# Kernel optimization log

Measured on AMD Instinct MI355X. Metric: run time of the kernel, lower is better.

Reference implementation:

```python
import jax, jax.numpy as jnp
import numpy as np

HEAD_SIZE = 64
BLOCK_SIZE = 4096
BATCH = 4


def setup_inputs() -> dict:
    key = jax.random.key(0)
    kx, kk, kq, kv = jax.random.split(key, 4)
    x = jax.random.normal(kx, (BATCH, BLOCK_SIZE, HEAD_SIZE), dtype=jnp.float32)
    s = HEAD_SIZE ** -0.5  # ~ torch default linear init scale
    Wk = jax.random.uniform(kk, (HEAD_SIZE, HEAD_SIZE), jnp.float32, -s, s)
    Wq = jax.random.uniform(kq, (HEAD_SIZE, HEAD_SIZE), jnp.float32, -s, s)
    Wv = jax.random.uniform(kv, (HEAD_SIZE, HEAD_SIZE), jnp.float32, -s, s)
    return {"x": x, "Wk": Wk, "Wq": Wq, "Wv": Wv}


def reference(x, Wk, Wq, Wv):
    # x: [B, T, C]; W*: [C, C] stored torch-style (out, in) -> y = x @ W.T
    B, T, C = x.shape
    k = x @ Wk.T  # [B, T, C]
    q = x @ Wq.T
    v = x @ Wv.T
    scores = jnp.einsum('btc,bsc->bts', q, k) * (C ** -0.5)  # [B, T, T]
    causal = jnp.tril(jnp.ones((T, T), dtype=bool))
    scores = jnp.where(causal, scores, -jnp.inf)
    weights = jax.nn.softmax(scores, axis=-1)
    out = jnp.einsum('bts,bsc->btc', weights, v)  # [B, T, C]
    return out
```

## Files before the change

### kernel.cpp

```cpp
#include <hip/hip_runtime.h>
#include <hip/hip_bf16.h>

typedef unsigned short u16;
typedef unsigned int u32;
typedef __bf16 bf16x8_t __attribute__((ext_vector_type(8)));
typedef float f32x4_t __attribute__((ext_vector_type(4)));
typedef float f32x16 __attribute__((ext_vector_type(16)));

constexpr int Bb = 4;
constexpr int Tt = 4096;
constexpr int Dd = 64;
constexpr float QSCALE = 0.18033688011112042f;

__device__ __forceinline__ u16 f2bf(float f) {
  unsigned int u = __builtin_bit_cast(unsigned int, f);
  return (u16)((u + 0x7fffu + ((u >> 16) & 1u)) >> 16);
}
__device__ __forceinline__ u32 pk2(float a, float b) {
  return (u32)f2bf(a) | ((u32)f2bf(b) << 16);
}
__device__ __forceinline__ u32 pkt(float a, float b) {
  const u32 ua = __builtin_bit_cast(u32, a);
  const u32 ub = __builtin_bit_cast(u32, b);
  return (ua >> 16) | (ub & 0xFFFF0000u);
}
__device__ __forceinline__ bf16x8_t ld16(const u16* p) {
  int4 v = *(const int4*)p;
  return __builtin_bit_cast(bf16x8_t, v);
}
__device__ __forceinline__ f32x4_t mfma16(bf16x8_t a, bf16x8_t b, f32x4_t c) {
  return __builtin_amdgcn_mfma_f32_16x16x32_bf16(a, b, c, 0, 0, 0);
}
__device__ __forceinline__ f32x16 mfma32(bf16x8_t a, bf16x8_t b, f32x16 c) {
  return __builtin_amdgcn_mfma_f32_32x32x16_bf16(a, b, c, 0, 0, 0);
}

__global__ __launch_bounds__(256) void HeadV1_proj(
    const float* __restrict__ x, const float* __restrict__ Wk,
    const float* __restrict__ Wq, const float* __restrict__ Wv,
    u16* __restrict__ qS, u16* __restrict__ kS, u16* __restrict__ vS)
{
  __shared__ u16 xl[64][72];
  __shared__ u16 Wl[3][64][72];
  __shared__ u16 ylds[64][72];

  const int t = threadIdx.x;
  const int w = t >> 6, lane = t & 63, l15 = lane & 15, quad = lane >> 4;
  const int r0 = blockIdx.x * 64;
  const int b  = r0 >> 12;
  const int kt = (r0 & 4095) >> 6;
  const long tilebase = ((long)(b * 64 + kt)) * 4096;

  {
    const float* srcs[4] = {x + (long)r0 * 64, Wk, Wq, Wv};
    u16* dstl[4] = {&xl[0][0], &Wl[0][0][0], &Wl[1][0][0], &Wl[2][0][0]};
    #pragma unroll
    for (int mm = 0; mm < 4; mm++) {
      const float* s = srcs[mm];
      u16* d = dstl[mm];
      #pragma unroll
      for (int i = 0; i < 4; i++) {
        const int f4 = i * 256 + t;
        const int row = f4 >> 4, c4 = f4 & 15;
        float4 v = ((const float4*)(s + row * 64))[c4];
        uint2 pk;
        pk.x = pk2(v.x, v.y);
        pk.y = pk2(v.z, v.w);
        *(uint2*)(d + row * 72 + c4 * 4) = pk;
      }
    }
  }
  __syncthreads();

  bf16x8_t xf[2];
  #pragma unroll
  for (int kh = 0; kh < 2; kh++)
    xf[kh] = ld16(&xl[w * 16 + l15][kh * 32 + quad * 8]);

  u16* dsts[3];
  dsts[0] = kS + tilebase; dsts[1] = qS + tilebase; dsts[2] = vS + tilebase;

  #pragma unroll
  for (int m = 0; m < 3; m++) {
    float vals[4][4];
    #pragma unroll
    for (int g = 0; g < 4; g++) {
      f32x4_t acc = {0.f, 0.f, 0.f, 0.f};
      #pragma unroll
      for (int kh = 0; kh < 2; kh++) {
        bf16x8_t wf = ld16(&Wl[m][g * 16 + l15][kh * 32 + quad * 8]);
        acc = mfma16(xf[kh], wf, acc);
      }
      #pragma unroll
      for (int r = 0; r < 4; r++)
        vals[g][r] = (m == 1) ? acc[r] * QSCALE : acc[r];
    }
    #pragma unroll
    for (int g = 0; g < 4; g++)
      #pragma unroll
      for (int r = 0; r < 4; r++)
        ylds[w * 16 + quad * 4 + r][g * 16 + l15] = f2bf(vals[g][r]);
    __syncthreads();
    if (m < 2) {
      #pragma unroll
      for (int kk = 0; kk < 2; kk++) {
        bf16x8_t f = ld16(&ylds[w * 16 + l15][kk * 32 + quad * 8]);
        *(int4*)(dsts[m] + (w * 2 + kk) * 512 + lane * 8) = __builtin_bit_cast(int4, f);
      }
    } else {
      #pragma unroll
      for (int kk = 0; kk < 2; kk++) {
        u16 tmp[8];
        #pragma unroll
        for (int j = 0; j < 8; j++)
          tmp[j] = ylds[kk * 32 + quad * 8 + j][w * 16 + l15];
        *(int4*)(dsts[2] + (kk * 4 + w) * 512 + lane * 8) = *(const int4*)tmp;
      }
    }
    __syncthreads();
  }
}

__global__ __launch_bounds__(1024, 4) void HeadV1_flash(
    const u16* __restrict__ qS, const u16* __restrict__ kS,
    const u16* __restrict__ vS, float* __restrict__ outg)
{
  __shared__ __align__(16) char smem[55296];
  float (*chk)[16][33]  = (float (*)[16][33])smem;
  float (*stg)[32][68]  = (float (*)[32][68])(smem + 33792);
  float (*lst)[2][32]   = (float (*)[2][32])(smem + 51200);

  const int t    = threadIdx.x;
  const int w    = t >> 6;
  const int lane = t & 63;
  const int l15  = lane & 15;
  const int lhb  = lane >> 5;
  const int l4   = (lane >> 4) & 1;
  const int q31  = lane & 31;

  const int xcd = blockIdx.x & 7;
  const int b   = xcd >> 1;
  const int i   = ((blockIdx.x >> 3) << 1) | (xcd & 1);
  const int j1 = i, j2 = 127 - i;
  const int nk1 = (j1 >> 1) + 1;
  const int nk2 = (j2 >> 1) + 1;
  int n1 = (16 * nk1 + 32) / 65;
  if (n1 < 1) n1 = 1;
  if (n1 > 15) n1 = 15;

  const bool grp2 = (w >= n1);
  const int j   = grp2 ? j2 : j1;
  const int nk  = grp2 ? nk2 : nk1;
  const int str = grp2 ? (16 - n1) : n1;
  const int off = grp2 ? (w - n1) : w;

  const int qt64 = j >> 1;
  const int ql0  = (j & 1) * 32;
  const int qr0  = j * 32;
  const long base = (long)b * Tt * Dd;

  const u16* qt_ = qS + ((long)(b * 64 + qt64)) * 4096;
  bf16x8_t qfrag[4];
  #pragma unroll
  for (int dsl = 0; dsl < 4; dsl++)
    qfrag[dsl] = ld16(qt_ + (((ql0 >> 4) + l4) * 2 + (dsl >> 1)) * 512
                          + (((dsl * 2 + lhb) & 3) * 16 + l15) * 8);

  f32x16 O0 = {0.f,0.f,0.f,0.f,0.f,0.f,0.f,0.f,0.f,0.f,0.f,0.f,0.f,0.f,0.f,0.f};
  f32x16 O1 = O0;
  float Lp = 0.f;

  const u16* kb = kS + ((long)(b * 64)) * 4096;
  const u16* vb = vS + ((long)(b * 64)) * 4096;

  for (int kt = off; kt < nk; kt += str) {
    const bool ismask = (kt == nk - 1);
    const u16* ktile = kb + (long)kt * 4096;
    const u16* vtile = vb + (long)kt * 4096;
    const int nh = (ismask && !(j & 1)) ? 1 : 2;

    for (int h2 = 0; h2 < nh; h2++) {
      bf16x8_t kf[4];
      #pragma unroll
      for (int dsl = 0; dsl < 4; dsl++)
        kf[dsl] = ld16(ktile + ((h2 * 2 + l4) * 2 + (dsl >> 1)) * 512
                             + (((dsl * 2 + lhb) & 3) * 16 + l15) * 8);
      bf16x8_t vf[2][2];
      #pragma unroll
      for (int ksl = 0; ksl < 2; ksl++)
        #pragma unroll
        for (int dh = 0; dh < 2; dh++)
          vf[ksl][dh] = ld16(vtile + (h2 * 4 + dh * 2 + l4) * 512
                                   + ((ksl * 2 + lhb) * 16 + l15) * 8);

      f32x16 S = {0.f,0.f,0.f,0.f,0.f,0.f,0.f,0.f,0.f,0.f,0.f,0.f,0.f,0.f,0.f,0.f};
      #pragma unroll
      for (int dsl = 0; dsl < 4; dsl++)
        S = mfma32(kf[dsl], qfrag[dsl], S);

      if (ismask && h2 == (j & 1)) {
        const int kvb = kt * 64 + h2 * 32 + 4 * lhb;
        const int qi  = qr0 + q31;
        #pragma unroll
        for (int r = 0; r < 16; r++) {
          const int kvg = kvb + (r & 3) + 8 * (r >> 2);
          if (kvg > qi) S[r] = -1e30f;
        }
      }

      float p[16];
      #pragma unroll
      for (int r = 0; r < 16; r++) p[r] = __builtin_amdgcn_exp2f(S[r]);
      #pragma unroll
      for (int r = 0; r < 16; r++) {
        const u32 u = __builtin_bit_cast(u32, p[r]) & 0xFFFF0000u;
        Lp += __builtin_bit_cast(float, u);
      }

      #pragma unroll
      for (int ksl = 0; ksl < 2; ksl++) {
        const u32 a0 = pkt(p[8 * ksl + 0], p[8 * ksl + 1]);
        const u32 a1 = pkt(p[8 * ksl + 2], p[8 * ksl + 3]);
        const u32 a2 = pkt(p[8 * ksl + 4], p[8 * ksl + 5]);
        const u32 a3 = pkt(p[8 * ksl + 6], p[8 * ksl + 7]);
        const u32 x02 = (u32)__shfl_xor((int)(lhb ? a0 : a2), 32);
        const u32 x13 = (u32)__shfl_xor((int)(lhb ? a1 : a3), 32);
        uint4 bw;
        bw.x = lhb ? x02 : a0;
        bw.y = lhb ? x13 : a1;
        bw.z = lhb ? a2 : x02;
        bw.w = lhb ? a3 : x13;
        const bf16x8_t Bf = __builtin_bit_cast(bf16x8_t, bw);
        __builtin_amdgcn_s_setprio(1);
        O0 = mfma32(vf[ksl][0], Bf, O0);
        O1 = mfma32(vf[ksl][1], Bf, O1);
        __builtin_amdgcn_s_setprio(0);
      }
    }
  }

  lst[w][lhb][q31] = Lp;
  __syncthreads();

  #pragma unroll
  for (int rr = 0; rr < 4; rr++) {
    #pragma unroll
    for (int rs = 0; rs < 8; rs++) {
      const int dloc = (rs & 3) + 8 * (rs >> 2) + 4 * lhb;
      const float val = (rr >> 1) ? ((rr & 1) ? O1[8 + rs] : O1[rs])
                                  : ((rr & 1) ? O0[8 + rs] : O0[rs]);
      chk[w][dloc][q31] = val;
    }
    __syncthreads();
    {
      const int jsel = t >> 9, tt = t & 511;
      const int d2 = tt >> 5, q = tt & 31;
      const int lo = jsel ? n1 : 0, hi = jsel ? 16 : n1;
      float s = 0.f;
      for (int w2 = lo; w2 < hi; w2++) s += chk[w2][d2][q];
      stg[jsel][q][rr * 16 + d2] = s;
    }
    __syncthreads();
  }

  {
    const int jsel = t >> 9, tt = t & 511;
    const int q = tt >> 4, dg = tt & 15;
    const int lo = jsel ? n1 : 0, hi = jsel ? 16 : n1;
    float L = 0.f;
    for (int w2 = lo; w2 < hi; w2++) L += lst[w2][0][q] + lst[w2][1][q];
    const float invL = 1.0f / L;
    const int jj = jsel ? j2 : j1;
    float4 v = *(const float4*)&stg[jsel][q][dg * 4];
    v.x *= invL; v.y *= invL; v.z *= invL; v.w *= invL;
    *(float4*)(outg + base + (long)(jj * 32 + q) * 64 + dg * 4) = v;
  }
}

extern "C" void kernel_launch(void* const* d_in, const int* in_sizes, int n_in,
                              void* d_out, int out_size, void* d_ws, size_t ws_size,
                              hipStream_t stream) {
  (void)in_sizes; (void)n_in; (void)out_size; (void)ws_size;
  const float* x  = (const float*)d_in[0];
  const float* Wk = (const float*)d_in[1];
  const float* Wq = (const float*)d_in[2];
  const float* Wv = (const float*)d_in[3];
  float* out = (float*)d_out;
  u16* qw  = (u16*)d_ws;
  u16* kw  = qw + (size_t)Bb * Tt * Dd;
  u16* vw  = kw + (size_t)Bb * Tt * Dd;

  HeadV1_proj<<<(Bb * Tt) / 64, 256, 0, stream>>>(x, Wk, Wq, Wv, qw, kw, vw);
  HeadV1_flash<<<256, 1024, 0, stream>>>(qw, kw, vw, out);
}
```

Measured before the change: 83.13 us.

## Compute softmax row sums via MFMA with ones and parallelize projection across 12 waves

The flash kernel no longer accumulates the softmax denominator with per-element VALU adds. It runs an extra 32x32 MFMA of a bf16 ones matrix against the packed probability fragment, which yields row sums already reduced across lanes, and the final reduction reads only one half. The projection kernel now launches 1024 threads so that three groups of four waves compute K, Q and V in parallel, each into its own LDS tile, removing the serial loop over matrices and its barriers. The cost is one extra MFMA per ksl step in the hot loop, plus four idle waves and more LDS in the projection blocks.

```diff
diff --git a/kernel.cpp b/kernel.cpp
--- a/kernel.cpp
+++ b/kernel.cpp
@@ -35,89 +35,86 @@
   return __builtin_amdgcn_mfma_f32_32x32x16_bf16(a, b, c, 0, 0, 0);
 }
 
-__global__ __launch_bounds__(256) void HeadV1_proj(
+__global__ __launch_bounds__(1024) void HeadV1_proj(
     const float* __restrict__ x, const float* __restrict__ Wk,
     const float* __restrict__ Wq, const float* __restrict__ Wv,
     u16* __restrict__ qS, u16* __restrict__ kS, u16* __restrict__ vS)
 {
   __shared__ u16 xl[64][72];
   __shared__ u16 Wl[3][64][72];
-  __shared__ u16 ylds[64][72];
+  __shared__ u16 yl[3][64][72];
 
   const int t = threadIdx.x;
   const int w = t >> 6, lane = t & 63, l15 = lane & 15, quad = lane >> 4;
-  const int r0 = blockIdx.x * 64;
-  const int b  = r0 >> 12;
-  const int kt = (r0 & 4095) >> 6;
+  const int blk = blockIdx.x;
+  const int r0 = blk * 64;
+  const int b  = blk >> 6;
+  const int kt = blk & 63;
   const long tilebase = ((long)(b * 64 + kt)) * 4096;
 
   {
     const float* srcs[4] = {x + (long)r0 * 64, Wk, Wq, Wv};
     u16* dstl[4] = {&xl[0][0], &Wl[0][0][0], &Wl[1][0][0], &Wl[2][0][0]};
+    const int row = t >> 4, c4 = t & 15;
     #pragma unroll
     for (int mm = 0; mm < 4; mm++) {
-      const float* s = srcs[mm];
-      u16* d = dstl[mm];
-      #pragma unroll
-      for (int i = 0; i < 4; i++) {
-        const int f4 = i * 256 + t;
-        const int row = f4 >> 4, c4 = f4 & 15;
-        float4 v = ((const float4*)(s + row * 64))[c4];
-        uint2 pk;
-        pk.x = pk2(v.x, v.y);
-        pk.y = pk2(v.z, v.w);
-        *(uint2*)(d + row * 72 + c4 * 4) = pk;
-      }
+      float4 v = ((const float4*)(srcs[mm] + row * 64))[c4];
+      uint2 pk;
+      pk.x = pk2(v.x, v.y);
+      pk.y = pk2(v.z, v.w);
+      *(uint2*)(dstl[mm] + row * 72 + c4 * 4) = pk;
     }
   }
   __syncthreads();
 
-  bf16x8_t xf[2];
-  #pragma unroll
-  for (int kh = 0; kh < 2; kh++)
-    xf[kh] = ld16(&xl[w * 16 + l15][kh * 32 + quad * 8]);
-
-  u16* dsts[3];
-  dsts[0] = kS + tilebase; dsts[1] = qS + tilebase; dsts[2] = vS + tilebase;
-
-  #pragma unroll
-  for (int m = 0; m < 3; m++) {
+  const int mg = w >> 2;
+  const int wl = w & 3;
+  if (mg < 3) {
+    bf16x8_t xf[2];
+    #pragma unroll
+    for (int kh = 0; kh < 2; kh++)
+      xf[kh] = ld16(&xl[wl * 16 + l15][kh * 32 + quad * 8]);
+
     float vals[4][4];
     #pragma unroll
     for (int g = 0; g < 4; g++) {
       f32x4_t acc = {0.f, 0.f, 0.f, 0.f};
       #pragma unroll
       for (int kh = 0; kh < 2; kh++) {
-        bf16x8_t wf = ld16(&Wl[m][g * 16 + l15][kh * 32 + quad * 8]);
+        bf16x8_t wf = ld16(&Wl[mg][g * 16 + l15][kh * 32 + quad * 8]);
         acc = mfma16(xf[kh], wf, acc);
       }
       #pragma unroll
       for (int r = 0; r < 4; r++)
-        vals[g][r] = (m == 1) ? acc[r] * QSCALE : acc[r];
+        vals[g][r] = (mg == 1) ? acc[r] * QSCALE : acc[r];
     }
     #pragma unroll
     for (int g = 0; g < 4; g++)
       #pragma unroll
       for (int r = 0; r < 4; r++)
-        ylds[w * 16 + quad * 4 + r][g * 16 + l15] = f2bf(vals[g][r]);
-    __syncthreads();
-    if (m < 2) {
+        yl[mg][wl * 16 + quad * 4 + r][g * 16 + l15] = f2bf(vals[g][r]);
+  }
+  __syncthreads();
+
+  if (mg < 3) {
+    u16* dsts[3];
+    dsts[0] = kS + tilebase; dsts[1] = qS + tilebase; dsts[2] = vS + tilebase;
+    if (mg < 2) {
       #pragma unroll
       for (int kk = 0; kk < 2; kk++) {
-        bf16x8_t f = ld16(&ylds[w * 16 + l15][kk * 32 + quad * 8]);
-        *(int4*)(dsts[m] + (w * 2 + kk) * 512 + lane * 8) = __builtin_bit_cast(int4, f);
+        bf16x8_t f = ld16(&yl[mg][wl * 16 + l15][kk * 32 + quad * 8]);
+        *(int4*)(dsts[mg] + (wl * 2 + kk) * 512 + lane * 8) = __builtin_bit_cast(int4, f);
       }
     } else {
       #pragma unroll
       for (int kk = 0; kk < 2; kk++) {
         u16 tmp[8];
         #pragma unroll
-        for (int j = 0; j < 8; j++)
-          tmp[j] = ylds[kk * 32 + quad * 8 + j][w * 16 + l15];
-        *(int4*)(dsts[2] + (kk * 4 + w) * 512 + lane * 8) = *(const int4*)tmp;
-      }
-    }
-    __syncthreads();
+        for (int jj = 0; jj < 8; jj++)
+          tmp[jj] = yl[2][kk * 32 + quad * 8 + jj][wl * 16 + l15];
+        *(int4*)(dsts[2] + (kk * 4 + wl) * 512 + lane * 8) = *(const int4*)tmp;
+      }
+    }
   }
 }
 
@@ -159,6 +156,10 @@
   const int qr0  = j * 32;
   const long base = (long)b * Tt * Dd;
 
+  union { u32 u4[4]; bf16x8_t v; } uo;
+  uo.u4[0] = uo.u4[1] = uo.u4[2] = uo.u4[3] = 0x3F803F80u;
+  const bf16x8_t ones = uo.v;
+
   const u16* qt_ = qS + ((long)(b * 64 + qt64)) * 4096;
   bf16x8_t qfrag[4];
   #pragma unroll
@@ -168,7 +169,7 @@
 
   f32x16 O0 = {0.f,0.f,0.f,0.f,0.f,0.f,0.f,0.f,0.f,0.f,0.f,0.f,0.f,0.f,0.f,0.f};
   f32x16 O1 = O0;
-  float Lp = 0.f;
+  f32x16 Lacc = O0;
 
   const u16* kb = kS + ((long)(b * 64)) * 4096;
   const u16* vb = vS + ((long)(b * 64)) * 4096;
@@ -208,21 +209,16 @@
         }
       }
 
-      float p[16];
-      #pragma unroll
-      for (int r = 0; r < 16; r++) p[r] = __builtin_amdgcn_exp2f(S[r]);
-      #pragma unroll
-      for (int r = 0; r < 16; r++) {
-        const u32 u = __builtin_bit_cast(u32, p[r]) & 0xFFFF0000u;
-        Lp += __builtin_bit_cast(float, u);
-      }
-
       #pragma unroll
       for (int ksl = 0; ksl < 2; ksl++) {
-        const u32 a0 = pkt(p[8 * ksl + 0], p[8 * ksl + 1]);
-        const u32 a1 = pkt(p[8 * ksl + 2], p[8 * ksl + 3]);
-        const u32 a2 = pkt(p[8 * ksl + 4], p[8 * ksl + 5]);
-        const u32 a3 = pkt(p[8 * ksl + 6], p[8 * ksl + 7]);
+        const u32 a0 = pkt(__builtin_amdgcn_exp2f(S[8 * ksl + 0]),
+                           __builtin_amdgcn_exp2f(S[8 * ksl + 1]));
+        const u32 a1 = pkt(__builtin_amdgcn_exp2f(S[8 * ksl + 2]),
+                           __builtin_amdgcn_exp2f(S[8 * ksl + 3]));
+        const u32 a2 = pkt(__builtin_amdgcn_exp2f(S[8 * ksl + 4]),
+                           __builtin_amdgcn_exp2f(S[8 * ksl + 5]));
+        const u32 a3 = pkt(__builtin_amdgcn_exp2f(S[8 * ksl + 6]),
+                           __builtin_amdgcn_exp2f(S[8 * ksl + 7]));
         const u32 x02 = (u32)__shfl_xor((int)(lhb ? a0 : a2), 32);
         const u32 x13 = (u32)__shfl_xor((int)(lhb ? a1 : a3), 32);
         uint4 bw;
@@ -231,6 +227,7 @@
         bw.z = lhb ? a2 : x02;
         bw.w = lhb ? a3 : x13;
         const bf16x8_t Bf = __builtin_bit_cast(bf16x8_t, bw);
+        Lacc = mfma32(ones, Bf, Lacc);
         __builtin_amdgcn_s_setprio(1);
         O0 = mfma32(vf[ksl][0], Bf, O0);
         O1 = mfma32(vf[ksl][1], Bf, O1);
@@ -239,7 +236,7 @@
     }
   }
 
-  lst[w][lhb][q31] = Lp;
+  lst[w][lhb][q31] = Lacc[0];
   __syncthreads();
 
   #pragma unroll
@@ -268,7 +265,7 @@
     const int q = tt >> 4, dg = tt & 15;
     const int lo = jsel ? n1 : 0, hi = jsel ? 16 : n1;
     float L = 0.f;
-    for (int w2 = lo; w2 < hi; w2++) L += lst[w2][0][q] + lst[w2][1][q];
+    for (int w2 = lo; w2 < hi; w2++) L += lst[w2][0][q];
     const float invL = 1.0f / L;
     const int jj = jsel ? j2 : j1;
     float4 v = *(const float4*)&stg[jsel][q][dg * 4];
@@ -290,6 +287,6 @@
   u16* kw  = qw + (size_t)Bb * Tt * Dd;
   u16* vw  = kw + (size_t)Bb * Tt * Dd;
 
-  HeadV1_proj<<<(Bb * Tt) / 64, 256, 0, stream>>>(x, Wk, Wq, Wv, qw, kw, vw);
+  HeadV1_proj<<<(Bb * Tt) / 64, 1024, 0, stream>>>(x, Wk, Wq, Wv, qw, kw, vw);
   HeadV1_flash<<<256, 1024, 0, stream>>>(qw, kw, vw, out);
 }
```

Measured after the change: 82.92 us. About the same (-0.3%).
